# Kernel optimization log

Measured on AMD Instinct MI355X. Metric: run time of the kernel, lower is better.

Reference implementation:

```python
import jax, jax.numpy as jnp
import numpy as np

B, IN, MEM, CTX, H = 8192, 1024, 1024, 1024, 4
DH = CTX // H

def setup_inputs() -> dict:
    key = jax.random.key(0)
    ks = jax.random.split(key, 20)
    s = 0.02
    d = {
        'input_tensor': jax.random.normal(ks[0], (B, IN), jnp.float32),
        'previous_memory': jax.random.normal(ks[1], (B, MEM), jnp.float32),
        # MultiheadAttention packed in_proj (q,k,v) and out_proj
        'in_proj_w': jax.random.normal(ks[2], (3 * CTX, CTX), jnp.float32) * s,
        'in_proj_b': jnp.zeros((3 * CTX,), jnp.float32),
        'out_proj_w': jax.random.normal(ks[3], (CTX, CTX), jnp.float32) * s,
        'out_proj_b': jnp.zeros((CTX,), jnp.float32),
        # input/memory projections
        'ip_w': jax.random.normal(ks[4], (CTX, IN), jnp.float32) * s,
        'ip_b': jnp.zeros((CTX,), jnp.float32),
        'mp_w': jax.random.normal(ks[5], (CTX, MEM), jnp.float32) * s,
        'mp_b': jnp.zeros((CTX,), jnp.float32),
        # forget / output gates
        'fg_w': jax.random.normal(ks[6], (MEM, MEM + IN), jnp.float32) * s,
        'fg_b': jnp.zeros((MEM,), jnp.float32),
        'og_w': jax.random.normal(ks[7], (MEM, MEM), jnp.float32) * s,
        'og_b': jnp.zeros((MEM,), jnp.float32),
        # GRUCell weights (PyTorch layout: [3*hidden, in], gates order r,z,n)
        'gru_w_ih': jax.random.normal(ks[8], (3 * MEM, CTX), jnp.float32) * s,
        'gru_b_ih': jnp.zeros((3 * MEM,), jnp.float32),
        'gru_w_hh': jax.random.normal(ks[9], (3 * MEM, MEM), jnp.float32) * s,
        'gru_b_hh': jnp.zeros((3 * MEM,), jnp.float32),
    }
    return d

def _forward(input_tensor, previous_memory, in_proj_w, in_proj_b, out_proj_w, out_proj_b,
             ip_w, ip_b, mp_w, mp_b, fg_w, fg_b, og_w, og_b,
             gru_w_ih, gru_b_ih, gru_w_hh, gru_b_hh):
    # projections
    pi = input_tensor @ ip_w.T + ip_b          # [B, CTX] (query; also context/value)
    pm = previous_memory @ mp_w.T + mp_b       # [B, CTX] (key)
    # MHA with q_len = kv_len = 1: softmax over a single key -> weights = 1
    wq, wk, wv = jnp.split(in_proj_w, 3, axis=0)
    bq, bk, bv = jnp.split(in_proj_b, 3, axis=0)
    q = (pi @ wq.T + bq).reshape(B, H, DH)
    k = (pm @ wk.T + bk).reshape(B, H, DH)
    v = (pi @ wv.T + bv).reshape(B, H, DH)
    scores = jnp.sum(q * k, axis=-1, keepdims=True) / jnp.sqrt(jnp.float32(DH))  # [B,H,1]
    w = jax.nn.softmax(scores, axis=-1)        # all ones (single key)
    attn = (w * v).reshape(B, CTX)             # == v
    context_aware = attn @ out_proj_w.T + out_proj_b  # [B, CTX]
    attention_weights = jnp.mean(w, axis=1)[:, None, :]  # [B,1,1], avg over heads
    # forget gate
    forget_in = jnp.concatenate([previous_memory, input_tensor], axis=-1)
    fgate = jax.nn.sigmoid(forget_in @ fg_w.T + fg_b)
    gated_mem = previous_memory * fgate
    # GRUCell (PyTorch semantics)
    gi = context_aware @ gru_w_ih.T + gru_b_ih
    gh = gated_mem @ gru_w_hh.T + gru_b_hh
    gi_r, gi_z, gi_n = jnp.split(gi, 3, axis=-1)
    gh_r, gh_z, gh_n = jnp.split(gh, 3, axis=-1)
    r = jax.nn.sigmoid(gi_r + gh_r)
    z = jax.nn.sigmoid(gi_z + gh_z)
    n = jnp.tanh(gi_n + r * gh_n)
    updated = (1.0 - z) * n + z * gated_mem
    ogate = jax.nn.sigmoid(updated @ og_w.T + og_b)
    return updated * ogate, attention_weights

def reference(input_tensor, previous_memory, in_proj_w, in_proj_b, out_proj_w, out_proj_b,
              ip_w, ip_b, mp_w, mp_b, fg_w, fg_b, og_w, og_b,
              gru_w_ih, gru_b_ih, gru_w_hh, gru_b_hh):
    return _forward(input_tensor, previous_memory, in_proj_w, in_proj_b, out_proj_w, out_proj_b,
                    ip_w, ip_b, mp_w, mp_b, fg_w, fg_b, og_w, og_b,
                    gru_w_ih, gru_b_ih, gru_w_hh, gru_b_hh)
```

## Files before the change

kernel.cpp:

```cpp
#include <hip/hip_runtime.h>
#include <cstdint>
#include <cstddef>


typedef __bf16 bf16;
typedef bf16 bf16x4 __attribute__((ext_vector_type(4)));
typedef bf16 bf16x8 __attribute__((ext_vector_type(8)));
typedef float f32x4 __attribute__((ext_vector_type(4)));

#define B_ROWS 8192

__device__ __forceinline__ float sigmoid_f(float x) {
    return 1.0f / (1.0f + __expf(-x));
}
__device__ __forceinline__ float tanh_f(float x) {
    return 1.0f - 2.0f / (__expf(2.0f * x) + 1.0f);
}

template <int BM>
__device__ __forceinline__ void gemm_core_db(
    bf16* sA, bf16* sB,
    const bf16* __restrict__ A, int lda,
    const bf16* __restrict__ W, int ldw,
    const float* __restrict__ bias,
    int N, int K, int brow, int bcol, int epi,
    bf16* __restrict__ out_bf, float* __restrict__ out_f32,
    const float* __restrict__ aux_f32, const bf16* __restrict__ aux_bf,
    int tld)
{
    constexpr int AI = BM / 32;
    const int tid  = threadIdx.x;
    const int lane = tid & 63;
    const int wave = tid >> 6;
    const int wr   = (wave & 1) * (BM / 2);
    const int wc   = (wave >> 1) * 64;
    const int lrow = lane & 15;
    const int lq   = lane >> 4;

    f32x4 acc[AI][4];
#pragma unroll
    for (int i = 0; i < AI; ++i)
#pragma unroll
        for (int j = 0; j < 4; ++j) {
            f32x4 z = {0.0f, 0.0f, 0.0f, 0.0f};
            acc[i][j] = z;
        }

    auto stage = [&](int sel, int k0) {
#pragma unroll
        for (int i = 0; i < BM / 64; ++i) {
            const int s   = tid + i * 256;
            const int row = s >> 2;
            const int col = (((s & 3) ^ ((s >> 3) & 3)) << 3);
            const bf16* gp = A + (size_t)(brow + row) * lda + (k0 + col);
            __builtin_amdgcn_global_load_lds(
                (const __attribute__((address_space(1))) void*)gp,
                (__attribute__((address_space(3))) void*)(&sA[sel * (BM * 32) + s * 8]),
                16, 0, 0);
        }
#pragma unroll
        for (int i = 0; i < 2; ++i) {
            const int s   = tid + i * 256;
            const int row = s >> 2;
            const int col = (((s & 3) ^ ((s >> 3) & 3)) << 3);
            const bf16* gp = W + (size_t)(bcol + row) * ldw + (k0 + col);
            __builtin_amdgcn_global_load_lds(
                (const __attribute__((address_space(1))) void*)gp,
                (__attribute__((address_space(3))) void*)(&sB[sel * 4096 + s * 8]),
                16, 0, 0);
        }
    };

    const int NT = K >> 5;

    stage(0, 0);
    asm volatile("s_waitcnt vmcnt(0)" ::: "memory");
    __builtin_amdgcn_s_barrier();
    __builtin_amdgcn_sched_barrier(0);

    for (int kt = 0; kt < NT; ++kt) {
        const int cur = kt & 1;
        bf16* cA = sA + cur * (BM * 32);
        bf16* cB = sB + cur * 4096;

        bf16x8 av[AI], bv[4];
#pragma unroll
        for (int i = 0; i < AI; ++i) {
            const int r = wr + i * 16 + lrow;
            av[i] = *(const bf16x8*)&cA[r * 32 + ((lq ^ ((r >> 1) & 3)) << 3)];
        }
#pragma unroll
        for (int j = 0; j < 4; ++j) {
            const int r = wc + j * 16 + lrow;
            bv[j] = *(const bf16x8*)&cB[r * 32 + ((lq ^ ((r >> 1) & 3)) << 3)];
        }

        if (kt + 1 < NT) stage(cur ^ 1, (kt + 1) << 5);

#pragma unroll
        for (int i = 0; i < AI; ++i)
#pragma unroll
            for (int j = 0; j < 4; ++j)
                acc[i][j] = __builtin_amdgcn_mfma_f32_16x16x32_bf16(
                    av[i], bv[j], acc[i][j], 0, 0, 0);

        __builtin_amdgcn_sched_barrier(0);
        asm volatile("s_waitcnt vmcnt(0) lgkmcnt(0)" ::: "memory");
        __builtin_amdgcn_s_barrier();
        __builtin_amdgcn_sched_barrier(0);
    }

#pragma unroll
    for (int j = 0; j < 4; ++j) {
        const int gcol = bcol + wc + j * 16 + lrow;
        const float bj = bias ? bias[gcol] : 0.0f;
#pragma unroll
        for (int i = 0; i < AI; ++i) {
            const int growb = brow + wr + i * 16 + lq * 4;
#pragma unroll
            for (int r = 0; r < 4; ++r) {
                const int grow = growb + r;
                const float val = acc[i][j][r] + bj;
                if (epi == 0) {
                    out_bf[(size_t)grow * N + gcol] = (bf16)val;
                } else if (epi == 1) {
                    const size_t idx = (size_t)grow * N + gcol;
                    out_bf[idx] = (bf16)(aux_f32[idx] * sigmoid_f(val));
                } else if (epi == 2) {
                    const size_t idx = (size_t)grow * N + gcol;
                    out_f32[idx] = (float)aux_bf[idx] * sigmoid_f(val);
                } else {
                    out_bf[(size_t)gcol * tld + grow] = (bf16)val;
                }
            }
        }
    }
}

__global__ __launch_bounds__(256, 2) void gemm128_k(
    const bf16* __restrict__ A, int lda, const bf16* __restrict__ W, int ldw,
    const float* __restrict__ bias, int N, int K, int epi,
    bf16* __restrict__ out_bf, float* __restrict__ out_f32,
    const float* __restrict__ aux_f32, const bf16* __restrict__ aux_bf,
    int tld, int nby)
{
    __shared__ bf16 sA[2 * 128 * 32];
    __shared__ bf16 sB[2 * 128 * 32];
    const int by = blockIdx.x % nby;
    const int bx = blockIdx.x / nby;
    gemm_core_db<128>(sA, sB, A, lda, W, ldw, bias, N, K,
                      by * 128, bx * 128, epi,
                      out_bf, out_f32, aux_f32, aux_bf, tld);
}

__global__ __launch_bounds__(256, 2) void gemm64_k(
    const bf16* __restrict__ A, int lda, const bf16* __restrict__ W, int ldw,
    const float* __restrict__ bias, int N, int K, int epi,
    bf16* __restrict__ out_bf, float* __restrict__ out_f32,
    const float* __restrict__ aux_f32, const bf16* __restrict__ aux_bf,
    int tld, int nby)
{
    __shared__ bf16 sA[2 * 64 * 32];
    __shared__ bf16 sB[2 * 128 * 32];
    const int by = blockIdx.x % nby;
    const int bx = blockIdx.x / nby;
    gemm_core_db<64>(sA, sB, A, lda, W, ldw, bias, N, K,
                     by * 64, bx * 128, epi,
                     out_bf, out_f32, aux_f32, aux_bf, tld);
}


__global__ void cast_weights_k(
    const float* __restrict__ wv, const float* __restrict__ wop,
    const float* __restrict__ wih, const float* __restrict__ wfg,
    const float* __restrict__ wog,
    bf16* __restrict__ dv, bf16* __restrict__ dop, bf16* __restrict__ dih,
    bf16* __restrict__ dfg, bf16* __restrict__ dog)
{
    int c = blockIdx.x * 256 + threadIdx.x;
    const float* s;
    bf16* d;
    int o;
    if (c < 262144)        { s = wv;  d = dv;  o = c; }
    else if (c < 524288)   { s = wop; d = dop; o = c - 262144; }
    else if (c < 1310720)  { s = wih; d = dih; o = c - 524288; }
    else if (c < 1835008)  { s = wfg; d = dfg; o = c - 1310720; }
    else                   { s = wog; d = dog; o = c - 1835008; }
    f32x4 v = ((const f32x4*)s)[o];
    bf16x4 t = {(bf16)v[0], (bf16)v[1], (bf16)v[2], (bf16)v[3]};
    ((bf16x4*)d)[o] = t;
}

__global__ void cast_f32_bf16_k(const float* __restrict__ src,
                                bf16* __restrict__ dst, int n4) {
    int i = blockIdx.x * 256 + threadIdx.x;
    if (i >= n4) return;
    f32x4 v = ((const f32x4*)src)[i];
    bf16x4 o = {(bf16)v[0], (bf16)v[1], (bf16)v[2], (bf16)v[3]};
    ((bf16x4*)dst)[i] = o;
}

__global__ void build_cat_k(const float* __restrict__ mem,
                            const float* __restrict__ inp,
                            bf16* __restrict__ cat) {
    int i = blockIdx.x * 256 + threadIdx.x;
    int row = i >> 9;
    int c4  = i & 511;
    f32x4 v;
    if (c4 < 256)
        v = ((const f32x4*)mem)[(size_t)row * 256 + c4];
    else
        v = ((const f32x4*)inp)[(size_t)row * 256 + (c4 - 256)];
    bf16x4 o = {(bf16)v[0], (bf16)v[1], (bf16)v[2], (bf16)v[3]};
    ((bf16x4*)cat)[i] = o;
}

__global__ void transpose_cast_k(const float* __restrict__ src,
                                 bf16* __restrict__ dst, int R, int C) {
    __shared__ float t[32][33];
    int bx = blockIdx.x * 32;
    int by = blockIdx.y * 32;
    int tx = threadIdx.x & 31, ty = threadIdx.x >> 5;
#pragma unroll
    for (int i = 0; i < 32; i += 8)
        t[ty + i][tx] = src[(size_t)(by + ty + i) * C + bx + tx];
    __syncthreads();
#pragma unroll
    for (int i = 0; i < 32; i += 8)
        dst[(size_t)(bx + ty + i) * R + by + tx] = (bf16)t[tx][ty + i];
}

__global__ void gemv_k(const float* __restrict__ W, const float* __restrict__ x,
                       const float* __restrict__ b, float* __restrict__ y,
                       int K) {
    int n    = blockIdx.x * 4 + (threadIdx.x >> 6);
    int lane = threadIdx.x & 63;
    const float* row = W + (size_t)n * K;
    float s = 0.0f;
    for (int k = lane * 4; k < K; k += 256) {
        f32x4 w = *(const f32x4*)(row + k);
        f32x4 xv = *(const f32x4*)(x + k);
        s += w[0] * xv[0] + w[1] * xv[1] + w[2] * xv[2] + w[3] * xv[3];
    }
#pragma unroll
    for (int off = 32; off; off >>= 1) s += __shfl_down(s, off);
    if (lane == 0) y[n] = s + b[n];
}

__global__ void gru_combine_k(const bf16* __restrict__ gi,
                              const bf16* __restrict__ gh,
                              bf16* __restrict__ gated) {
    int i   = blockIdx.x * 256 + threadIdx.x;
    int row = i >> 7;
    int c   = (i & 127) << 3;
    size_t b3 = (size_t)row * 3072 + c;
    size_t b1 = (size_t)row * 1024 + c;
    bf16x8 gir = *(const bf16x8*)(gi + b3);
    bf16x8 giz = *(const bf16x8*)(gi + b3 + 1024);
    bf16x8 gin = *(const bf16x8*)(gi + b3 + 2048);
    bf16x8 ghr = *(const bf16x8*)(gh + b3);
    bf16x8 ghz = *(const bf16x8*)(gh + b3 + 1024);
    bf16x8 ghn = *(const bf16x8*)(gh + b3 + 2048);
    bf16x8 g   = *(const bf16x8*)(gated + b1);
    bf16x8 o;
#pragma unroll
    for (int e = 0; e < 8; ++e) {
        float r = sigmoid_f((float)gir[e] + (float)ghr[e]);
        float z = sigmoid_f((float)giz[e] + (float)ghz[e]);
        float n = tanh_f((float)gin[e] + r * (float)ghn[e]);
        o[e] = (bf16)((1.0f - z) * n + z * (float)g[e]);
    }
    *(bf16x8*)(gated + b1) = o;
}

__global__ void fill_ones_k(float* __restrict__ p, int n) {
    int i = blockIdx.x * 256 + threadIdx.x;
    if (i < n) p[i] = 1.0f;
}

extern "C" void kernel_launch(void* const* d_in, const int* in_sizes, int n_in,
                              void* d_out, int out_size, void* d_ws,
                              size_t ws_size, hipStream_t stream) {
    const float* input      = (const float*)d_in[0];
    const float* prev       = (const float*)d_in[1];
    const float* in_proj_w  = (const float*)d_in[2];
    const float* in_proj_b  = (const float*)d_in[3];
    const float* out_proj_w = (const float*)d_in[4];
    const float* out_proj_b = (const float*)d_in[5];
    const float* ip_w       = (const float*)d_in[6];
    const float* ip_b       = (const float*)d_in[7];
    const float* fg_w  = (const float*)d_in[10];
    const float* fg_b  = (const float*)d_in[11];
    const float* og_w  = (const float*)d_in[12];
    const float* og_b  = (const float*)d_in[13];
    const float* gih_w = (const float*)d_in[14];
    const float* gih_b = (const float*)d_in[15];
    const float* ghh_w = (const float*)d_in[16];
    const float* ghh_b = (const float*)d_in[17];
    float* out = (float*)d_out;

    char* ws = (char*)d_ws;
    const size_t MB = 1024 * 1024;
    bf16* CAT   = (bf16*)(ws);
    bf16* WHHB  = (bf16*)(ws);
    bf16* GI    = (bf16*)(ws + 32 * MB);
    bf16* GH    = (bf16*)(ws + 80 * MB);
    bf16* WVB   = (bf16*)(ws + 80 * MB);
    bf16* WOPB  = (bf16*)(ws + 82 * MB);
    bf16* WIHB  = (bf16*)(ws + 84 * MB);
    bf16* WIPT  = (bf16*)(ws + 90 * MB);
    bf16* T1T   = (bf16*)(ws + 92 * MB);
    bf16* T2T   = (bf16*)(ws + 94 * MB);
    bf16* WFGB  = (bf16*)(ws + 96 * MB);
    float* T1B  = (float*)(ws + 100 * MB);
    float* T2B  = (float*)(ws + 100 * MB + 8192);
    float* T3B  = (float*)(ws + 100 * MB + 16384);
    bf16* GATED = (bf16*)(ws + 128 * MB);
    bf16* WCOMB = (bf16*)(ws + 144 * MB);
    bf16* WOGB  = (bf16*)(ws + 150 * MB);

    const int M = B_ROWS;
    dim3 blk(256);

    build_cat_k<<<dim3((M * 2048 / 4) / 256), blk, 0, stream>>>(prev, input, CAT);
    cast_weights_k<<<dim3(8192), blk, 0, stream>>>(
        in_proj_w + 2048 * 1024, out_proj_w, gih_w, fg_w, og_w,
        WVB, WOPB, WIHB, WFGB, WOGB);
    transpose_cast_k<<<dim3(32, 32), blk, 0, stream>>>(ip_w, WIPT, 1024, 1024);
    gemv_k<<<dim3(256), blk, 0, stream>>>(in_proj_w + 2048 * 1024, ip_b, in_proj_b + 2048, T1B, 1024);
    gemv_k<<<dim3(256), blk, 0, stream>>>(out_proj_w, T1B, out_proj_b, T2B, 1024);
    gemv_k<<<dim3(768), blk, 0, stream>>>(gih_w, T2B, gih_b, T3B, 1024);
    gemm64_k<<<dim3(128), blk, 0, stream>>>(WVB, 1024, WIPT, 1024, nullptr,
        1024, 1024, 3, T1T, nullptr, nullptr, nullptr, 1024, 16);
    gemm64_k<<<dim3(128), blk, 0, stream>>>(WOPB, 1024, T1T, 1024, nullptr,
        1024, 1024, 3, T2T, nullptr, nullptr, nullptr, 1024, 16);
    gemm64_k<<<dim3(384), blk, 0, stream>>>(WIHB, 1024, T2T, 1024, nullptr,
        1024, 1024, 0, WCOMB, nullptr, nullptr, nullptr, 0, 48);
    gemm128_k<<<dim3(512), blk, 0, stream>>>(CAT, 2048, WFGB, 2048,
        fg_b, 1024, 2048, 1, GATED, nullptr, prev, nullptr, 0, 64);
    gemm128_k<<<dim3(1536), blk, 0, stream>>>(CAT + 1024, 2048, WCOMB,
        1024, T3B, 3072, 1024, 0, GI, nullptr, nullptr, nullptr, 0, 64);
    cast_f32_bf16_k<<<dim3(3072), blk, 0, stream>>>(ghh_w, WHHB, 3072 * 1024 / 4);
    gemm128_k<<<dim3(1536), blk, 0, stream>>>(GATED, 1024, WHHB, 1024,
        ghh_b, 3072, 1024, 0, GH, nullptr, nullptr, nullptr, 0, 64);
    gru_combine_k<<<dim3(M * 1024 / 8 / 256), blk, 0, stream>>>(GI, GH, GATED);
    gemm128_k<<<dim3(512), blk, 0, stream>>>(GATED, 1024, WOGB, 1024,
        og_b, 1024, 1024, 2, nullptr, out, nullptr, GATED, 0, 64);
    fill_ones_k<<<dim3(32), blk, 0, stream>>>(out + (size_t)M * 1024, M);
}
```

Measured before the change: 524.6 us.

## Triple-buffer GEMM LDS staging with partial vmcnt waits

Replaces the double-buffered global-to-LDS pipeline with a three-stage ring, prefetching two K-tiles ahead. Each iteration waits only for the older tile's loads (partial vmcnt) instead of draining all outstanding loads. The goal is to hide global memory latency behind MFMA work. In exchange, LDS use per block rises, which could limit occupancy, and the final iterations issue redundant loads of the last tile.

```diff
diff --git a/kernel.cpp b/kernel.cpp
--- a/kernel.cpp
+++ b/kernel.cpp
@@ -18,7 +18,7 @@
 }
 
 template <int BM>
-__device__ __forceinline__ void gemm_core_db(
+__device__ __forceinline__ void gemm_core_tb(
     bf16* sA, bf16* sB,
     const bf16* __restrict__ A, int lda,
     const bf16* __restrict__ W, int ldw,
@@ -46,7 +46,7 @@
             acc[i][j] = z;
         }
 
-    auto stage = [&](int sel, int k0) {
+    auto stage = [&](bf16* dA, bf16* dB, int k0) {
 #pragma unroll
         for (int i = 0; i < BM / 64; ++i) {
             const int s   = tid + i * 256;
@@ -55,7 +55,7 @@
             const bf16* gp = A + (size_t)(brow + row) * lda + (k0 + col);
             __builtin_amdgcn_global_load_lds(
                 (const __attribute__((address_space(1))) void*)gp,
-                (__attribute__((address_space(3))) void*)(&sA[sel * (BM * 32) + s * 8]),
+                (__attribute__((address_space(3))) void*)(&dA[s * 8]),
                 16, 0, 0);
         }
 #pragma unroll
@@ -66,36 +66,46 @@
             const bf16* gp = W + (size_t)(bcol + row) * ldw + (k0 + col);
             __builtin_amdgcn_global_load_lds(
                 (const __attribute__((address_space(1))) void*)gp,
-                (__attribute__((address_space(3))) void*)(&sB[sel * 4096 + s * 8]),
+                (__attribute__((address_space(3))) void*)(&dB[s * 8]),
                 16, 0, 0);
         }
     };
 
+#define WAIT_LPS()                                                   \
+    do {                                                             \
+        if constexpr (BM == 128)                                     \
+            asm volatile("s_waitcnt vmcnt(4)" ::: "memory");         \
+        else                                                         \
+            asm volatile("s_waitcnt vmcnt(3)" ::: "memory");         \
+    } while (0)
+
     const int NT = K >> 5;
 
-    stage(0, 0);
-    asm volatile("s_waitcnt vmcnt(0)" ::: "memory");
+    bf16* a0 = sA;               bf16* b0 = sB;
+    bf16* a1 = sA + BM * 32;     bf16* b1 = sB + 4096;
+    bf16* a2 = sA + 2 * BM * 32; bf16* b2 = sB + 2 * 4096;
+
+    stage(a0, b0, 0);
+    stage(a1, b1, NT > 1 ? 32 : 0);
+    WAIT_LPS();
     __builtin_amdgcn_s_barrier();
     __builtin_amdgcn_sched_barrier(0);
 
     for (int kt = 0; kt < NT; ++kt) {
-        const int cur = kt & 1;
-        bf16* cA = sA + cur * (BM * 32);
-        bf16* cB = sB + cur * 4096;
-
         bf16x8 av[AI], bv[4];
 #pragma unroll
         for (int i = 0; i < AI; ++i) {
             const int r = wr + i * 16 + lrow;
-            av[i] = *(const bf16x8*)&cA[r * 32 + ((lq ^ ((r >> 1) & 3)) << 3)];
+            av[i] = *(const bf16x8*)&a0[r * 32 + ((lq ^ ((r >> 1) & 3)) << 3)];
         }
 #pragma unroll
         for (int j = 0; j < 4; ++j) {
             const int r = wc + j * 16 + lrow;
-            bv[j] = *(const bf16x8*)&cB[r * 32 + ((lq ^ ((r >> 1) & 3)) << 3)];
-        }
-
-        if (kt + 1 < NT) stage(cur ^ 1, (kt + 1) << 5);
+            bv[j] = *(const bf16x8*)&b0[r * 32 + ((lq ^ ((r >> 1) & 3)) << 3)];
+        }
+
+        const int kn = (kt + 2 < NT ? kt + 2 : NT - 1) << 5;
+        stage(a2, b2, kn);
 
 #pragma unroll
         for (int i = 0; i < AI; ++i)
@@ -105,10 +115,16 @@
                     av[i], bv[j], acc[i][j], 0, 0, 0);
 
         __builtin_amdgcn_sched_barrier(0);
-        asm volatile("s_waitcnt vmcnt(0) lgkmcnt(0)" ::: "memory");
+        WAIT_LPS();
         __builtin_amdgcn_s_barrier();
         __builtin_amdgcn_sched_barrier(0);
+
+        bf16* ta = a0; a0 = a1; a1 = a2; a2 = ta;
+        bf16* tb = b0; b0 = b1; b1 = b2; b2 = tb;
     }
+
+    asm volatile("s_waitcnt vmcnt(0)" ::: "memory");
+#undef WAIT_LPS
 
 #pragma unroll
     for (int j = 0; j < 4; ++j) {
@@ -144,11 +160,11 @@
     const float* __restrict__ aux_f32, const bf16* __restrict__ aux_bf,
     int tld, int nby)
 {
-    __shared__ bf16 sA[2 * 128 * 32];
-    __shared__ bf16 sB[2 * 128 * 32];
+    __shared__ bf16 sA[3 * 128 * 32];
+    __shared__ bf16 sB[3 * 128 * 32];
     const int by = blockIdx.x % nby;
     const int bx = blockIdx.x / nby;
-    gemm_core_db<128>(sA, sB, A, lda, W, ldw, bias, N, K,
+    gemm_core_tb<128>(sA, sB, A, lda, W, ldw, bias, N, K,
                       by * 128, bx * 128, epi,
                       out_bf, out_f32, aux_f32, aux_bf, tld);
 }
@@ -160,11 +176,11 @@
     const float* __restrict__ aux_f32, const bf16* __restrict__ aux_bf,
     int tld, int nby)
 {
-    __shared__ bf16 sA[2 * 64 * 32];
-    __shared__ bf16 sB[2 * 128 * 32];
+    __shared__ bf16 sA[3 * 64 * 32];
+    __shared__ bf16 sB[3 * 128 * 32];
     const int by = blockIdx.x % nby;
     const int bx = blockIdx.x / nby;
-    gemm_core_db<64>(sA, sB, A, lda, W, ldw, bias, N, K,
+    gemm_core_tb<64>(sA, sB, A, lda, W, ldw, bias, N, K,
                      by * 64, bx * 128, epi,
                      out_bf, out_f32, aux_f32, aux_bf, tld);
 }
```

After: 531.8 us. About the same (+1.4%).
